# Optimization experiments

Measured on AMD Instinct MI355X. Metric: run time of the kernel, lower is better.

## Reference

```python
import jax, jax.numpy as jnp
import numpy as np

B, N, F_IN, F_OUT = 8, 2048, 64, 64
NEG = -9.0e15  # matches torch's -9000000000000000.0 mask value


def setup_inputs() -> dict:
    key = jax.random.key(0)
    ks = jax.random.split(key, 12)
    stdv1 = 1.0 / np.sqrt(F_IN)
    stdv2 = 1.0 / np.sqrt(2 * F_OUT)
    x = jax.random.normal(ks[0], (B, N, F_IN), dtype=jnp.float32)
    adj = jax.random.randint(ks[1], (B, N, N), 0, 2).astype(jnp.int32)
    identity = jnp.broadcast_to(jnp.eye(N, dtype=jnp.int32), (B, N, N))
    def unif(k, shape, s):
        return jax.random.uniform(k, shape, jnp.float32, -s, s)
    return {
        "x": x, "adj": adj, "identity": identity,
        "W1": unif(ks[2], (F_OUT, F_IN), stdv1), "b1": unif(ks[3], (F_OUT,), stdv1),
        "a1": unif(ks[4], (1, 2 * F_OUT), stdv2), "ab1": unif(ks[5], (1,), stdv2),
        "W2": unif(ks[6], (F_OUT, F_IN), stdv1), "b2": unif(ks[7], (F_OUT,), stdv1),
        "a2": unif(ks[8], (1, 2 * F_OUT), stdv2), "ab2": unif(ks[9], (1,), stdv2),
    }


def _gat_layer(x, mask, W, b, a, ab):
    # linear1
    h = jnp.einsum('bnf,of->bno', x, W) + b                     # [B,N,Fo]
    Fo = h.shape[-1]
    # linear2 on concat(h_i, h_j) decomposes: e_ij = relu(h_i.a1 + h_j.a2 + ab)
    s1 = h @ a[0, :Fo]                                          # [B,N]
    s2 = h @ a[0, Fo:]                                          # [B,N]
    e = jax.nn.relu(s1[:, :, None] + s2[:, None, :] + ab[0])    # [B,N,N]
    e = jnp.where(mask > 0, e, NEG)
    att = jax.nn.softmax(e, axis=2)                             # [B,N,N]
    return jnp.einsum('bnm,bmf->bnf', att, h)                   # dropout p=0 / eval


def reference(x, adj, identity, W1, b1, a1, ab1, W2, b2, a2, ab2):
    out1 = _gat_layer(x, adj, W1, b1, a1, ab1)
    out2 = _gat_layer(x, identity, W2, b2, a2, ab2)
    return out1 + out2
```

## Files before the change

### kernel.cpp

```cpp
#include <hip/hip_runtime.h>


#define DEVI __device__ __forceinline__

typedef __attribute__((ext_vector_type(8))) short short8;
typedef __attribute__((ext_vector_type(4))) float floatx4;

DEVI unsigned short f2bf(float x) {
    unsigned u = __builtin_bit_cast(unsigned, x);
    unsigned r = u + 0x7FFFu + ((u >> 16) & 1u);
    return (unsigned short)(r >> 16);
}

DEVI short8 pack8(const float* v) {
    short8 r;
#pragma unroll
    for (int i = 0; i < 8; ++i) r[i] = (short)f2bf(v[i]);
    return r;
}

DEVI unsigned cvt_pk_bf16(float lo, float hi) {
    unsigned r;
    asm("v_cvt_pk_bf16_f32 %0, %1, %2" : "=v"(r) : "v"(lo), "v"(hi));
    return r;
}

__global__ __launch_bounds__(256) void k_prep(
    const float* __restrict__ x, const float* __restrict__ W1,
    const float* __restrict__ b1, const float* __restrict__ a1,
    const float* __restrict__ ab1,
    unsigned short* __restrict__ hT1,
    float* __restrict__ t1,
    float* __restrict__ s2a)
{
    __shared__ __align__(16) unsigned short hstage[64][72];
    const int tid = threadIdx.x;
    const int w = tid >> 6, lane = tid & 63;
    const int g = lane >> 4, r15 = lane & 15;
    const int blockRow = blockIdx.x * 64;
    const int rowbase = blockRow + w * 16;

    float xa[8], xb[8];
    const float* xrow = x + (long)(rowbase + r15) * 64;
#pragma unroll
    for (int e = 0; e < 8; ++e) { xa[e] = xrow[g * 8 + e]; xb[e] = xrow[32 + g * 8 + e]; }
    short8 A0 = pack8(xa), A1 = pack8(xb);

    floatx4 acc[4];
#pragma unroll
    for (int nt = 0; nt < 4; ++nt) {
        float wa[8], wb[8];
        const float* wrow = W1 + (nt * 16 + r15) * 64;
#pragma unroll
        for (int e = 0; e < 8; ++e) { wa[e] = wrow[g * 8 + e]; wb[e] = wrow[32 + g * 8 + e]; }
        short8 B0 = pack8(wa), B1 = pack8(wb);
        floatx4 c = {0.f, 0.f, 0.f, 0.f};
        c = __builtin_amdgcn_mfma_f32_16x16x32_bf16(A0, B0, c, 0, 0, 0);
        c = __builtin_amdgcn_mfma_f32_16x16x32_bf16(A1, B1, c, 0, 0, 0);
        float bias = b1[nt * 16 + r15];
#pragma unroll
        for (int q = 0; q < 4; ++q) c[q] += bias;
        acc[nt] = c;
    }

    float a1lo[4], a1hi[4];
#pragma unroll
    for (int nt = 0; nt < 4; ++nt) {
        a1lo[nt] = a1[nt * 16 + r15];
        a1hi[nt] = a1[64 + nt * 16 + r15];
    }
    float s1q[4], s2q[4];
#pragma unroll
    for (int q = 0; q < 4; ++q) {
        float s1 = 0.f, s2 = 0.f;
#pragma unroll
        for (int nt = 0; nt < 4; ++nt) { s1 += acc[nt][q] * a1lo[nt]; s2 += acc[nt][q] * a1hi[nt]; }
#pragma unroll
        for (int m = 1; m < 16; m <<= 1) { s1 += __shfl_xor(s1, m); s2 += __shfl_xor(s2, m); }
        s1q[q] = s1; s2q[q] = s2;
    }
    if (r15 == 0) {
        float abv = ab1[0];
#pragma unroll
        for (int q = 0; q < 4; ++q) {
            t1[rowbase + 4 * g + q] = s1q[q] + abv;
            s2a[rowbase + 4 * g + q] = s2q[q];
        }
    }

#pragma unroll
    for (int nt = 0; nt < 4; ++nt)
#pragma unroll
        for (int q = 0; q < 4; ++q)
            hstage[nt * 16 + r15][w * 16 + 4 * g + q] = f2bf(acc[nt][q]);
    __syncthreads();
    {
        const int o = tid >> 2, seg = (tid & 3) * 16;
        const int bb = blockRow >> 11;
        const int ib = blockRow & 2047;
        unsigned short* dst = hT1 + ((long)(bb * 64 + o) * 2048) + ib + seg;
        uint4 v0 = *(const uint4*)&hstage[o][seg];
        uint4 v1 = *(const uint4*)&hstage[o][seg + 8];
        *(uint4*)dst = v0;
        *(uint4*)(dst + 8) = v1;
    }
}

__global__ __launch_bounds__(512) void k_attn(
    const float* __restrict__ x, const int* __restrict__ adj,
    const float* __restrict__ W2, const float* __restrict__ b2,
    const unsigned short* __restrict__ hT1,
    const float* __restrict__ t1, const float* __restrict__ s2a,
    float* __restrict__ out)
{
    __shared__ __align__(16) unsigned short hl[2][2][64][72];
    __shared__ __align__(16) unsigned short plds[8][16][72];
    __shared__ __align__(16) float accbuf[4][64][16];
    __shared__ float ldenom[2][4][16];

    const int tid = threadIdx.x;
    const int w = tid >> 6, lane = tid & 63;
    const int t = w >> 2, wrow = w & 3;
    const int g = lane >> 4, r15 = lane & 15;
    const int jl = lane & 31, rh = lane >> 5;
    const int bb = blockIdx.x >> 5;
    const int i0 = (blockIdx.x & 31) * 64;
    const int rowbase = i0 + wrow * 16;
    const int jc0 = t * 16;

    float tr8[8];
#pragma unroll
    for (int r = 0; r < 8; ++r) tr8[r] = t1[bb * 2048 + rowbase + 8 * rh + r];
    float lpart[8];
#pragma unroll
    for (int r = 0; r < 8; ++r) lpart[r] = 0.f;
    floatx4 acc[4];
#pragma unroll
    for (int nt = 0; nt < 4; ++nt) acc[nt] = (floatx4){0.f, 0.f, 0.f, 0.f};

    const int ttid = tid & 255;
    const int so = ttid >> 2, sseg = (ttid & 3) * 16;
    const unsigned short* hTsrc = hT1 + (long)(bb * 64 + so) * 2048 + sseg;
    unsigned short* hldst0 = &hl[t][0][so][sseg];
    unsigned short* hldst1 = &hl[t][1][so][sseg];

    const int2* adjp = (const int2*)adj + (long)(bb * 2048 + rowbase + 8 * rh) * 1024 + jl;
    const float2* s2p = (const float2*)(s2a + bb * 2048) + jl;

#define LOADN(AJ, S2, H0, H1, itp) do {                                        \
        const int jcn_ = jc0 + (itp);                                          \
        H0 = *(const uint4*)(hTsrc + jcn_ * 64);                               \
        H1 = *(const uint4*)(hTsrc + jcn_ * 64 + 8);                           \
        _Pragma("unroll")                                                      \
        for (int r_ = 0; r_ < 8; ++r_) AJ[r_] = adjp[(long)r_ * 1024 + jcn_ * 32]; \
        S2 = s2p[jcn_ * 32];                                                   \
    } while (0)

#define COMPUTE(AJ, S2, buf) do {                                              \
        _Pragma("unroll")                                                      \
        for (int r_ = 0; r_ < 8; ++r_) {                                       \
            float z0 = tr8[r_] + S2.x, z1 = tr8[r_] + S2.y;                    \
            z0 = z0 > 0.f ? z0 : 0.f; z1 = z1 > 0.f ? z1 : 0.f;                \
            float p0 = AJ[r_].x > 0 ? __expf(z0) : 0.f;                        \
            float p1 = AJ[r_].y > 0 ? __expf(z1) : 0.f;                        \
            lpart[r_] += p0 + p1;                                              \
            *(unsigned*)&plds[w][8 * rh + r_][2 * jl] = cvt_pk_bf16(p0, p1);   \
        }                                                                      \
        short8 a0 = *(const short8*)&plds[w][r15][g * 8];                      \
        short8 a1 = *(const short8*)&plds[w][r15][32 + g * 8];                 \
        _Pragma("unroll")                                                      \
        for (int nt_ = 0; nt_ < 4; ++nt_) {                                    \
            short8 b0 = *(const short8*)&hl[t][buf][nt_ * 16 + r15][g * 8];    \
            short8 b1 = *(const short8*)&hl[t][buf][nt_ * 16 + r15][32 + g * 8]; \
            acc[nt_] = __builtin_amdgcn_mfma_f32_16x16x32_bf16(a0, b0, acc[nt_], 0, 0, 0); \
            acc[nt_] = __builtin_amdgcn_mfma_f32_16x16x32_bf16(a1, b1, acc[nt_], 0, 0, 0); \
        }                                                                      \
    } while (0)

    uint4 hA0, hA1, hB0, hB1;
    int2 adjA[8], adjB[8];
    float2 s2A, s2B;

    LOADN(adjA, s2A, hA0, hA1, 0);
    *(uint4*)hldst0 = hA0;
    *(uint4*)(hldst0 + 8) = hA1;

    for (int ith = 0; ith < 8; ++ith) {
        const int it = 2 * ith;
        __syncthreads();
        LOADN(adjB, s2B, hB0, hB1, it + 1);
        COMPUTE(adjA, s2A, 0);
        { *(uint4*)hldst1 = hB0; *(uint4*)(hldst1 + 8) = hB1; }

        __syncthreads();
        if (ith < 7) LOADN(adjA, s2A, hA0, hA1, it + 2);
        COMPUTE(adjB, s2B, 1);
        if (ith < 7) { *(uint4*)hldst0 = hA0; *(uint4*)(hldst0 + 8) = hA1; }
    }

    float red[8];
#pragma unroll
    for (int r = 0; r < 8; ++r) {
        float v = lpart[r];
#pragma unroll
        for (int m = 1; m < 32; m <<= 1) v += __shfl_xor(v, m);
        red[r] = v;
    }
    if (jl == 0) {
#pragma unroll
        for (int r = 0; r < 8; ++r) ldenom[t][wrow][8 * rh + r] = red[r];
    }
    if (t == 1) {
#pragma unroll
        for (int nt = 0; nt < 4; ++nt)
            *(floatx4*)&accbuf[wrow][lane][nt * 4] = acc[nt];
    }
    __syncthreads();

    if (t == 0) {
#pragma unroll
        for (int nt = 0; nt < 4; ++nt) {
            floatx4 pa = *(const floatx4*)&accbuf[wrow][lane][nt * 4];
#pragma unroll
            for (int q = 0; q < 4; ++q) acc[nt][q] += pa[q];
        }
        float linv[4];
#pragma unroll
        for (int q = 0; q < 4; ++q) {
            float d = ldenom[0][wrow][4 * g + q] + ldenom[1][wrow][4 * g + q];
            linv[q] = 1.0f / d;
        }

        float xa[8], xb[8];
        const float* xrow = x + ((long)(bb * 2048 + rowbase + r15)) * 64;
#pragma unroll
        for (int e = 0; e < 8; ++e) { xa[e] = xrow[g * 8 + e]; xb[e] = xrow[32 + g * 8 + e]; }
        short8 A0 = pack8(xa), A1 = pack8(xb);
#pragma unroll
        for (int nt = 0; nt < 4; ++nt) {
            float wa[8], wb[8];
            const float* wrow2 = W2 + (nt * 16 + r15) * 64;
#pragma unroll
            for (int e = 0; e < 8; ++e) { wa[e] = wrow2[g * 8 + e]; wb[e] = wrow2[32 + g * 8 + e]; }
            short8 B0 = pack8(wa), B1 = pack8(wb);
            floatx4 c = {0.f, 0.f, 0.f, 0.f};
            c = __builtin_amdgcn_mfma_f32_16x16x32_bf16(A0, B0, c, 0, 0, 0);
            c = __builtin_amdgcn_mfma_f32_16x16x32_bf16(A1, B1, c, 0, 0, 0);
            float bias = b2[nt * 16 + r15];
#pragma unroll
            for (int q = 0; q < 4; ++q) {
                float val = acc[nt][q] * linv[q] + c[q] + bias;
                out[((long)(bb * 2048 + rowbase + 4 * g + q)) * 64 + nt * 16 + r15] = val;
            }
        }
    }
#undef LOADN
#undef COMPUTE
}

extern "C" void kernel_launch(void* const* d_in, const int* in_sizes, int n_in,
                              void* d_out, int out_size, void* d_ws, size_t ws_size,
                              hipStream_t stream) {
    const float* x   = (const float*)d_in[0];
    const int*   adj = (const int*)d_in[1];
    const float* W1  = (const float*)d_in[3];
    const float* b1  = (const float*)d_in[4];
    const float* a1  = (const float*)d_in[5];
    const float* ab1 = (const float*)d_in[6];
    const float* W2  = (const float*)d_in[7];
    const float* b2  = (const float*)d_in[8];

    unsigned short* hT1 = (unsigned short*)d_ws;
    float* t1  = (float*)((char*)d_ws + (size_t)8 * 64 * 2048 * 2);
    float* s2a = t1 + 8 * 2048;

    k_prep<<<256, 256, 0, stream>>>(x, W1, b1, a1, ab1, hT1, t1, s2a);
    k_attn<<<256, 512, 0, stream>>>(x, adj, W2, b2, hT1, t1, s2a, (float*)d_out);
}
```

Baseline: 40.22 us.

## Load attention B operands directly into registers, dropping LDS staging and barriers

The attention loop no longer stages hT1 tiles through shared memory. Each lane loads its MFMA B fragments straight from global memory, and P values are produced in a layout matching the MFMA A operand with wider int4/float4 adjacency loads. This removes per-iteration __syncthreads and LDS traffic. The x@W2 epilogue also moves to the t==1 waves so it overlaps with the final combine. In exchange, register pressure rises from the double-buffered fragments, and global loads become less coalesced since each lane reads strided 16-byte chunks of hT1.

```diff
diff --git a/kernel.cpp b/kernel.cpp
--- a/kernel.cpp
+++ b/kernel.cpp
@@ -113,124 +113,102 @@
     const float* __restrict__ t1, const float* __restrict__ s2a,
     float* __restrict__ out)
 {
-    __shared__ __align__(16) unsigned short hl[2][2][64][72];
     __shared__ __align__(16) unsigned short plds[8][16][72];
-    __shared__ __align__(16) float accbuf[4][64][16];
+    __shared__ __align__(16) float accbuf[4][16][64];
+    __shared__ __align__(16) float h2buf[4][16][64];
     __shared__ float ldenom[2][4][16];
 
     const int tid = threadIdx.x;
     const int w = tid >> 6, lane = tid & 63;
     const int t = w >> 2, wrow = w & 3;
     const int g = lane >> 4, r15 = lane & 15;
-    const int jl = lane & 31, rh = lane >> 5;
     const int bb = blockIdx.x >> 5;
     const int i0 = (blockIdx.x & 31) * 64;
     const int rowbase = i0 + wrow * 16;
-    const int jc0 = t * 16;
-
-    float tr8[8];
-#pragma unroll
-    for (int r = 0; r < 8; ++r) tr8[r] = t1[bb * 2048 + rowbase + 8 * rh + r];
-    float lpart[8];
-#pragma unroll
-    for (int r = 0; r < 8; ++r) lpart[r] = 0.f;
+    const int jbase = t * 16;
+
+    float tr4[4];
+#pragma unroll
+    for (int rr = 0; rr < 4; ++rr) tr4[rr] = t1[bb * 2048 + rowbase + rr * 4 + g];
+    float lpart[4];
+#pragma unroll
+    for (int rr = 0; rr < 4; ++rr) lpart[rr] = 0.f;
     floatx4 acc[4];
 #pragma unroll
     for (int nt = 0; nt < 4; ++nt) acc[nt] = (floatx4){0.f, 0.f, 0.f, 0.f};
 
-    const int ttid = tid & 255;
-    const int so = ttid >> 2, sseg = (ttid & 3) * 16;
-    const unsigned short* hTsrc = hT1 + (long)(bb * 64 + so) * 2048 + sseg;
-    unsigned short* hldst0 = &hl[t][0][so][sseg];
-    unsigned short* hldst1 = &hl[t][1][so][sseg];
-
-    const int2* adjp = (const int2*)adj + (long)(bb * 2048 + rowbase + 8 * rh) * 1024 + jl;
-    const float2* s2p = (const float2*)(s2a + bb * 2048) + jl;
-
-#define LOADN(AJ, S2, H0, H1, itp) do {                                        \
-        const int jcn_ = jc0 + (itp);                                          \
-        H0 = *(const uint4*)(hTsrc + jcn_ * 64);                               \
-        H1 = *(const uint4*)(hTsrc + jcn_ * 64 + 8);                           \
-        _Pragma("unroll")                                                      \
-        for (int r_ = 0; r_ < 8; ++r_) AJ[r_] = adjp[(long)r_ * 1024 + jcn_ * 32]; \
-        S2 = s2p[jcn_ * 32];                                                   \
+    const int4* adjq = (const int4*)(adj + (long)(bb * 2048 + rowbase + g) * 2048) + r15;
+    const float4* s2q = (const float4*)(s2a + (long)bb * 2048) + r15;
+    const unsigned short* hbase = hT1 + (long)(bb * 64 + r15) * 2048 + g * 8;
+
+    int4 adjA[4], adjB[4];
+    float4 A_s2, B_s2;
+    short8 b0A[4], b1A[4], b0B[4], b1B[4];
+
+#define LOADSET(S, c) do {                                                     \
+        const int jc_ = jbase + (c);                                           \
+        S##_s2 = s2q[jc_ * 16];                                                \
+        _Pragma("unroll")                                                      \
+        for (int rr_ = 0; rr_ < 4; ++rr_) adj##S[rr_] = adjq[rr_ * 2048 + jc_ * 16]; \
+        _Pragma("unroll")                                                      \
+        for (int nt_ = 0; nt_ < 4; ++nt_) {                                    \
+            b0##S[nt_] = *(const short8*)(hbase + nt_ * 32768 + jc_ * 64);     \
+            b1##S[nt_] = *(const short8*)(hbase + nt_ * 32768 + jc_ * 64 + 32);\
+        }                                                                      \
     } while (0)
 
-#define COMPUTE(AJ, S2, buf) do {                                              \
-        _Pragma("unroll")                                                      \
-        for (int r_ = 0; r_ < 8; ++r_) {                                       \
-            float z0 = tr8[r_] + S2.x, z1 = tr8[r_] + S2.y;                    \
-            z0 = z0 > 0.f ? z0 : 0.f; z1 = z1 > 0.f ? z1 : 0.f;                \
-            float p0 = AJ[r_].x > 0 ? __expf(z0) : 0.f;                        \
-            float p1 = AJ[r_].y > 0 ? __expf(z1) : 0.f;                        \
-            lpart[r_] += p0 + p1;                                              \
-            *(unsigned*)&plds[w][8 * rh + r_][2 * jl] = cvt_pk_bf16(p0, p1);   \
+#define COMPUTE(S) do {                                                        \
+        _Pragma("unroll")                                                      \
+        for (int rr_ = 0; rr_ < 4; ++rr_) {                                    \
+            float z0 = fmaxf(tr4[rr_] + S##_s2.x, 0.f);                        \
+            float z1 = fmaxf(tr4[rr_] + S##_s2.y, 0.f);                        \
+            float z2 = fmaxf(tr4[rr_] + S##_s2.z, 0.f);                        \
+            float z3 = fmaxf(tr4[rr_] + S##_s2.w, 0.f);                        \
+            float p0 = adj##S[rr_].x > 0 ? __expf(z0) : 0.f;                   \
+            float p1 = adj##S[rr_].y > 0 ? __expf(z1) : 0.f;                   \
+            float p2 = adj##S[rr_].z > 0 ? __expf(z2) : 0.f;                   \
+            float p3 = adj##S[rr_].w > 0 ? __expf(z3) : 0.f;                   \
+            lpart[rr_] += (p0 + p1) + (p2 + p3);                               \
+            uint2 u;                                                           \
+            u.x = cvt_pk_bf16(p0, p1);                                         \
+            u.y = cvt_pk_bf16(p2, p3);                                         \
+            *(uint2*)&plds[w][rr_ * 4 + g][r15 * 4] = u;                       \
         }                                                                      \
         short8 a0 = *(const short8*)&plds[w][r15][g * 8];                      \
         short8 a1 = *(const short8*)&plds[w][r15][32 + g * 8];                 \
         _Pragma("unroll")                                                      \
         for (int nt_ = 0; nt_ < 4; ++nt_) {                                    \
-            short8 b0 = *(const short8*)&hl[t][buf][nt_ * 16 + r15][g * 8];    \
-            short8 b1 = *(const short8*)&hl[t][buf][nt_ * 16 + r15][32 + g * 8]; \
-            acc[nt_] = __builtin_amdgcn_mfma_f32_16x16x32_bf16(a0, b0, acc[nt_], 0, 0, 0); \
-            acc[nt_] = __builtin_amdgcn_mfma_f32_16x16x32_bf16(a1, b1, acc[nt_], 0, 0, 0); \
+            acc[nt_] = __builtin_amdgcn_mfma_f32_16x16x32_bf16(a0, b0##S[nt_], acc[nt_], 0, 0, 0); \
+            acc[nt_] = __builtin_amdgcn_mfma_f32_16x16x32_bf16(a1, b1##S[nt_], acc[nt_], 0, 0, 0); \
         }                                                                      \
     } while (0)
 
-    uint4 hA0, hA1, hB0, hB1;
-    int2 adjA[8], adjB[8];
-    float2 s2A, s2B;
-
-    LOADN(adjA, s2A, hA0, hA1, 0);
-    *(uint4*)hldst0 = hA0;
-    *(uint4*)(hldst0 + 8) = hA1;
-
+    LOADSET(A, 0);
+    LOADSET(B, 1);
+#pragma unroll 2
     for (int ith = 0; ith < 8; ++ith) {
-        const int it = 2 * ith;
-        __syncthreads();
-        LOADN(adjB, s2B, hB0, hB1, it + 1);
-        COMPUTE(adjA, s2A, 0);
-        { *(uint4*)hldst1 = hB0; *(uint4*)(hldst1 + 8) = hB1; }
-
-        __syncthreads();
-        if (ith < 7) LOADN(adjA, s2A, hA0, hA1, it + 2);
-        COMPUTE(adjB, s2B, 1);
-        if (ith < 7) { *(uint4*)hldst0 = hA0; *(uint4*)(hldst0 + 8) = hA1; }
-    }
-
-    float red[8];
-#pragma unroll
-    for (int r = 0; r < 8; ++r) {
-        float v = lpart[r];
-#pragma unroll
-        for (int m = 1; m < 32; m <<= 1) v += __shfl_xor(v, m);
-        red[r] = v;
-    }
-    if (jl == 0) {
-#pragma unroll
-        for (int r = 0; r < 8; ++r) ldenom[t][wrow][8 * rh + r] = red[r];
-    }
+        COMPUTE(A);
+        if (ith < 7) LOADSET(A, 2 * ith + 2);
+        COMPUTE(B);
+        if (ith < 7) LOADSET(B, 2 * ith + 3);
+    }
+#undef LOADSET
+#undef COMPUTE
+
+#pragma unroll
+    for (int rr = 0; rr < 4; ++rr) {
+        float v = lpart[rr];
+#pragma unroll
+        for (int m = 1; m < 16; m <<= 1) v += __shfl_xor(v, m);
+        if (r15 == 0) ldenom[t][wrow][rr * 4 + g] = v;
+    }
+
     if (t == 1) {
 #pragma unroll
         for (int nt = 0; nt < 4; ++nt)
-            *(floatx4*)&accbuf[wrow][lane][nt * 4] = acc[nt];
-    }
-    __syncthreads();
-
-    if (t == 0) {
-#pragma unroll
-        for (int nt = 0; nt < 4; ++nt) {
-            floatx4 pa = *(const floatx4*)&accbuf[wrow][lane][nt * 4];
-#pragma unroll
-            for (int q = 0; q < 4; ++q) acc[nt][q] += pa[q];
-        }
-        float linv[4];
-#pragma unroll
-        for (int q = 0; q < 4; ++q) {
-            float d = ldenom[0][wrow][4 * g + q] + ldenom[1][wrow][4 * g + q];
-            linv[q] = 1.0f / d;
-        }
-
+#pragma unroll
+            for (int q = 0; q < 4; ++q)
+                accbuf[wrow][4 * g + q][nt * 16 + r15] = acc[nt][q];
         float xa[8], xb[8];
         const float* xrow = x + ((long)(bb * 2048 + rowbase + r15)) * 64;
 #pragma unroll
@@ -248,14 +226,26 @@
             c = __builtin_amdgcn_mfma_f32_16x16x32_bf16(A1, B1, c, 0, 0, 0);
             float bias = b2[nt * 16 + r15];
 #pragma unroll
+            for (int q = 0; q < 4; ++q)
+                h2buf[wrow][4 * g + q][nt * 16 + r15] = c[q] + bias;
+        }
+    }
+    __syncthreads();
+
+    if (t == 0) {
+        float linv[4];
+#pragma unroll
+        for (int q = 0; q < 4; ++q)
+            linv[q] = 1.0f / (ldenom[0][wrow][4 * g + q] + ldenom[1][wrow][4 * g + q]);
+#pragma unroll
+        for (int nt = 0; nt < 4; ++nt)
+#pragma unroll
             for (int q = 0; q < 4; ++q) {
-                float val = acc[nt][q] * linv[q] + c[q] + bias;
+                float total = acc[nt][q] + accbuf[wrow][4 * g + q][nt * 16 + r15];
+                float val = total * linv[q] + h2buf[wrow][4 * g + q][nt * 16 + r15];
                 out[((long)(bb * 2048 + rowbase + 4 * g + q)) * 64 + nt * 16 + r15] = val;
             }
-        }
-    }
-#undef LOADN
-#undef COMPUTE
+    }
 }
 
 extern "C" void kernel_launch(void* const* d_in, const int* in_sizes, int n_in,
```

Result: slower. 49.30 us (+22.6%).
